# Kernel tuning notes

Hardware: AMD Instinct MI355X
Metric: run time of the kernel (lower is better)

The kernel has to match this reference:

```python
import jax, jax.numpy as jnp
import numpy as np

H = 400   # hidden_size
V = 77    # vocab / window size
K = 10    # attention mixture components
OUT = 121
B, T, U = 64, 600, 50


def setup_inputs() -> dict:
    key = jax.random.key(0)
    ks = jax.random.split(key, 16)
    def p(k, shape, s=0.08):
        return jax.random.normal(k, shape, dtype=jnp.float32) * s
    # bias for kappa-increment chunk kept negative so kappa advances ~exp(-3)=0.05/step
    b_win = jnp.concatenate([jnp.zeros(2 * K, jnp.float32), jnp.full((K,), -3.0, jnp.float32)])
    return {
        "inputs": jax.random.normal(ks[0], (B, T, 3), dtype=jnp.float32),
        "text": jax.random.randint(ks[1], (B, U), 0, V),
        "text_mask": jnp.ones((B, U), jnp.float32),
        "h0": jnp.zeros((3, B, H), jnp.float32),
        "c0": jnp.zeros((3, B, H), jnp.float32),
        "prev_window_vec": jnp.zeros((B, 1, V), jnp.float32),
        "prev_kappa": jnp.zeros((B, K, 1), jnp.float32),
        "w_ih1": p(ks[2], (4 * H, 3 + V)), "w_hh1": p(ks[3], (4 * H, H)),
        "b_ih1": jnp.zeros((4 * H,), jnp.float32), "b_hh1": jnp.zeros((4 * H,), jnp.float32),
        "w_ih2": p(ks[4], (4 * H, 3 + V + H)), "w_hh2": p(ks[5], (4 * H, H)),
        "b_ih2": jnp.zeros((4 * H,), jnp.float32), "b_hh2": jnp.zeros((4 * H,), jnp.float32),
        "w_ih3": p(ks[6], (4 * H, 3 + V + H)), "w_hh3": p(ks[7], (4 * H, H)),
        "b_ih3": jnp.zeros((4 * H,), jnp.float32), "b_hh3": jnp.zeros((4 * H,), jnp.float32),
        "w_win": p(ks[8], (3 * K, H), 0.01), "b_win": b_win,
        "w_out": p(ks[9], (OUT, 3 * H)), "b_out": jnp.zeros((OUT,), jnp.float32),
    }


def lstm_cell(x, h, c, Wih, Whh, bih, bhh):
    # PyTorch gate order: i, f, g, o
    g = x @ Wih.T + bih + h @ Whh.T + bhh
    i, f, gg, o = jnp.split(g, 4, axis=-1)
    c = jax.nn.sigmoid(f) * c + jax.nn.sigmoid(i) * jnp.tanh(gg)
    h = jax.nn.sigmoid(o) * jnp.tanh(c)
    return h, c


def reference(inputs, text, text_mask, h0, c0, prev_window_vec, prev_kappa,
              w_ih1, w_hh1, b_ih1, b_hh1, w_ih2, w_hh2, b_ih2, b_hh2,
              w_ih3, w_hh3, b_ih3, b_hh3, w_win, b_win, w_out, b_out):
    enc = jax.nn.one_hot(text, V, dtype=jnp.float32)            # [B,U,V]
    u = jnp.arange(U, dtype=jnp.float32)                         # [U]

    def step1(carry, x_t):
        h, c, wv, kappa = carry                                  # h,c:[B,H] wv:[B,V] kappa:[B,K]
        xi = jnp.concatenate([x_t, wv], axis=-1)                 # [B,3+V]
        h, c = lstm_cell(xi, h, c, w_ih1, w_hh1, b_ih1, b_hh1)
        mix = jnp.exp(h @ w_win.T + b_win)                       # [B,3K]
        alpha, beta, dk = jnp.split(mix, 3, axis=-1)             # each [B,K]
        kappa = kappa + dk
        phi = jnp.sum(alpha[:, :, None] * jnp.exp(-beta[:, :, None] * (kappa[:, :, None] - u) ** 2), axis=1)  # [B,U]
        phi = phi * text_mask
        wv = jnp.einsum('bu,buv->bv', phi, enc)                  # [B,V]
        return (h, c, wv, kappa), (h, wv)

    carry0 = (h0[0], c0[0], prev_window_vec[:, 0, :], prev_kappa[:, :, 0])
    (h1, c1, _, kappa_last), (hid1, wvec) = jax.lax.scan(step1, carry0, jnp.swapaxes(inputs, 0, 1))
    hid1 = jnp.swapaxes(hid1, 0, 1)                              # [B,T,H]
    wvec = jnp.swapaxes(wvec, 0, 1)                              # [B,T,V]

    def run_lstm(x, h, c, Wih, Whh, bih, bhh):
        def step(carry, x_t):
            h, c = carry
            h, c = lstm_cell(x_t, h, c, Wih, Whh, bih, bhh)
            return (h, c), h
        _, hs = jax.lax.scan(step, (h, c), jnp.swapaxes(x, 0, 1))
        return jnp.swapaxes(hs, 0, 1)

    hid2 = run_lstm(jnp.concatenate([inputs, hid1, wvec], axis=-1), h0[1], c0[1], w_ih2, w_hh2, b_ih2, b_hh2)
    hid3 = run_lstm(jnp.concatenate([inputs, hid2, wvec], axis=-1), h0[2], c0[2], w_ih3, w_hh3, b_ih3, b_hh3)
    y_hat = jnp.concatenate([hid1, hid2, hid3], axis=-1) @ w_out.T + b_out  # [B,T,121]
    return y_hat, wvec, kappa_last[:, :, None]
```

## Files before the change

kernel.cpp:

```cpp
#include <hip/hip_runtime.h>
#include <cstdint>
#include <cstddef>
#include <cstring>

using u32 = unsigned int;
typedef _Float16 h2 __attribute__((ext_vector_type(2)));
typedef _Float16 h4 __attribute__((ext_vector_type(4)));
typedef _Float16 h8 __attribute__((ext_vector_type(8)));
typedef float f32x4 __attribute__((ext_vector_type(4)));

constexpr int B_=64, T_=600, U_=50, V_=77, H_=400, OUT_=121;
constexpr int G1=50, GPA=16, G2=50, G3=50, GOUT=8;
constexpr int NBLK = G1+GPA+G2+G3+GOUT;

constexpr size_t FLAGS_B = 0;
constexpr size_t FLAGS_SZ = 4ull*600*64*16;
constexpr size_t W1WG   = 15ull*32*4*8;
constexpr size_t W1F_B  = FLAGS_SZ;
constexpr size_t W2WG   = 28ull*32*4*8;
constexpr size_t W2F_B  = W1F_B + 50ull*W1WG*2;
constexpr size_t W3F_B  = W2F_B + 50ull*W2WG*2;
constexpr size_t WOWG   = 300ull*32*16;
constexpr size_t WOF_B  = W3F_B + 50ull*W2WG*2;
constexpr size_t WWFWG  = 200ull*32;
constexpr size_t WWF_B  = WOF_B + 8ull*WOWG*2;
constexpr size_t WWMWG  = 15ull*32*4*8;
constexpr size_t WWM_B  = WWF_B + 16ull*WWFWG*4;
constexpr size_t FWV_B  = WWM_B + 50ull*WWMWG*2;
constexpr size_t FH1_B  = FWV_B + 600ull*64*40*4;
constexpr size_t FH2_B  = FH1_B + 600ull*64*200*4;
constexpr size_t FH3_B  = FH2_B + 600ull*64*200*4;

constexpr int SW1 = 184;
constexpr int SW2 = 232;
constexpr int SWO = 244;
constexpr int SMEM_BYTES = 59392;

struct P {
  const float *x, *tmask, *h0, *c0, *pwv, *pkap;
  const int *text;
  const float *wih1,*whh1,*bih1,*bhh1;
  const float *wih2,*whh2,*bih2,*bhh2;
  const float *wih3,*whh3,*bih3,*bhh3;
  const float *wwin,*bwin,*wout,*bout;
  float *out_y,*out_wv,*out_kap;
  _Float16 *w1f,*w2f,*w3f,*wof,*wwm;
  u32 *wwf;
  u32 *fwv,*fh1,*fh2,*fh3;
  u32 *flags;
};

__device__ __forceinline__ u32 ldc_u(const u32* p) {
  return __hip_atomic_load((u32*)p, __ATOMIC_RELAXED, __HIP_MEMORY_SCOPE_AGENT);
}
__device__ __forceinline__ void stc_u(u32* p, u32 v) {
  __hip_atomic_store(p, v, __ATOMIC_RELAXED, __HIP_MEMORY_SCOPE_AGENT);
}
__device__ __forceinline__ float sigm(float x) { return 1.f/(1.f+__expf(-x)); }
__device__ __forceinline__ h2 pk16(float a, float b) {
  auto t = __builtin_amdgcn_cvt_pkrtz(a, b);
  h2 r; memcpy(&r, &t, 4); return r;
}
__device__ __forceinline__ u32 h2u(h2 v) { u32 r; memcpy(&r, &v, 4); return r; }
__device__ __forceinline__ h2 u2h(u32 v) { h2 r; memcpy(&r, &v, 4); return r; }
__device__ __forceinline__ u32 pkf(float a, float b) { return h2u(pk16(a, b)); }
__device__ __forceinline__ float dot2(h2 a, h2 b, float c) { return __builtin_amdgcn_fdot2(a, b, c, false); }
__device__ __forceinline__ h2 lo4(h4 v) { return __builtin_shufflevector(v, v, 0, 1); }
__device__ __forceinline__ h2 hi4(h4 v) { return __builtin_shufflevector(v, v, 2, 3); }

__device__ __forceinline__ void wait_flags(u32* f, int stage, int t, int n) {
  if ((int)threadIdx.x < n) {
    const u32* s = f + (((size_t)stage*600 + t)*64 + threadIdx.x)*4;
    while (ldc_u(s) == 0) __builtin_amdgcn_s_sleep(2);
  }
  __syncthreads();
}
__device__ __forceinline__ void set_flag(u32* f, int stage, int t, int prod) {
  if (threadIdx.x == 0)
    stc_u(f + (((size_t)stage*600 + t)*64 + prod)*4, 1u);
}

__device__ __forceinline__ void mfma_chunk5(const _Float16* pan, int SWf, const _Float16* WA,
                                            int w, int l, f32x4& acc0, f32x4& acc1) {
  const _Float16* bp0 = pan + ((w>>1)*32 + (l&15))*SWf + (l>>4)*8;
  const _Float16* bp1 = bp0 + 16*SWf;
  const _Float16* ap  = WA + (((16*(w&1) + (l&15))*4) + (l>>4))*8;
#pragma unroll
  for (int ks = 0; ks < 5; ++ks) {
    h8 a  = *(const h8*)(ap  + ks*1024);
    h8 b0 = *(const h8*)(bp0 + ks*32);
    h8 b1 = *(const h8*)(bp1 + ks*32);
    acc0 = __builtin_amdgcn_mfma_f32_16x16x32_f16(a, b0, acc0, 0, 0, 0);
    acc1 = __builtin_amdgcn_mfma_f32_16x16x32_f16(a, b1, acc1, 0, 0, 0);
  }
}
__device__ __forceinline__ void mfma_chunk7(const _Float16* pan, int SWf, const _Float16* WA,
                                            int w, int l, f32x4& acc0, f32x4& acc1) {
  const _Float16* bp0 = pan + ((w>>1)*32 + (l&15))*SWf + (l>>4)*8;
  const _Float16* bp1 = bp0 + 16*SWf;
  const _Float16* ap  = WA + (((16*(w&1) + (l&15))*4) + (l>>4))*8;
#pragma unroll
  for (int ks = 0; ks < 7; ++ks) {
    h8 a  = *(const h8*)(ap  + ks*1024);
    h8 b0 = *(const h8*)(bp0 + ks*32);
    h8 b1 = *(const h8*)(bp1 + ks*32);
    acc0 = __builtin_amdgcn_mfma_f32_16x16x32_f16(a, b0, acc0, 0, 0, 0);
    acc1 = __builtin_amdgcn_mfma_f32_16x16x32_f16(a, b1, acc1, 0, 0, 0);
  }
}

__device__ void lstm1_role(const P& p, int wg, char* smem) {
  const int tid = threadIdx.x;
  const int w = tid >> 6, l = tid & 63;
  const int ul = (w&1)*4 + (l>>4);
  const int u  = wg*8 + ul;
  const int bA = (w>>1)*32 + (l&15), bB = bA + 16;
  _Float16* panA = (_Float16*)smem;
  _Float16* panB = panA + 64*SW1;
  float* kapS = (float*)(smem + 47104);
  float* mixE = (float*)(smem + 49664);
  float* wvs  = (float*)(smem + 23552);
  _Float16* wgW = p.w1f + (size_t)wg * W1WG;
  _Float16* wgM = p.wwm + (size_t)wg * WWMWG;
  for (int e = tid; e < 15360; e += 256) {
    int i = e & 7, q = (e>>3)&3, row = (e>>5)&31, ks = e>>10;
    int k = ks*32 + q*8 + i;
    int cu = row>>2, g = row&3;
    int r = g*400 + wg*8 + cu;
    float v;
    if (k < 400)      v = p.whh1[(size_t)r*400 + k];
    else if (k < 477) v = p.wih1[(size_t)r*80 + 3 + (k-400)];
    else              v = p.wih1[(size_t)r*80 + (k-477)];
    wgW[e] = (_Float16)v;
  }
  for (int e = tid; e < 15360; e += 256) {
    int i = e & 7, q = (e>>3)&3, row = (e>>5)&31, ks = e>>10;
    int k = ks*32 + q*8 + i;
    float v = 0.f;
    if (row < 30 && k < 400) v = p.wwin[(size_t)row*400 + k];
    wgM[e] = (_Float16)v;
  }
  for (int i = tid; i < 640; i += 256) kapS[i] = p.pkap[i];
  float bsum[4];
#pragma unroll
  for (int g = 0; g < 4; ++g) bsum[g] = p.bih1[g*400+u] + p.bhh1[g*400+u];
  float creg[2];
  creg[0] = p.c0[(size_t)bA*H_ + u];
  creg[1] = p.c0[(size_t)bB*H_ + u];
  __syncthreads();

  for (int t = 0; t < T_; ++t) {
    f32x4 acc0 = {0.f,0.f,0.f,0.f}, acc1 = {0.f,0.f,0.f,0.f};
    f32x4 am0  = {0.f,0.f,0.f,0.f}, am1  = {0.f,0.f,0.f,0.f};
    if (t > 0) wait_flags(p.flags, 0, t-1, G1); else __syncthreads();
    const u32* h1p = p.fh1 + (size_t)(t-1)*64*200;
    {
      u32 tmp[20];
#pragma unroll
      for (int it = 0; it < 20; ++it) {
        int idx = tid + it*256; int b = idx/80, q = idx - b*80;
        if (t == 0) { float2 f = *(const float2*)(p.h0 + (size_t)b*H_ + 2*q); tmp[it] = pkf(f.x, f.y); }
        else tmp[it] = h1p[b*200 + q];
      }
#pragma unroll
      for (int it = 0; it < 20; ++it) {
        int idx = tid + it*256; int b = idx/80, q = idx - b*80;
        ((u32*)panA)[b*92 + q] = tmp[it];
      }
    }
    __syncthreads();
    {
      u32 tmp[20];
#pragma unroll
      for (int it = 0; it < 20; ++it) {
        int idx = tid + it*256; int b = idx/80, q = 80 + (idx - b*80);
        if (t == 0) { float2 f = *(const float2*)(p.h0 + (size_t)b*H_ + 2*q); tmp[it] = pkf(f.x, f.y); }
        else tmp[it] = h1p[b*200 + q];
      }
      mfma_chunk5(panA, SW1, wgW, w, l, acc0, acc1);
      if (t > 0) mfma_chunk5(panA, SW1, wgM, w, l, am0, am1);
#pragma unroll
      for (int it = 0; it < 20; ++it) {
        int idx = tid + it*256; int b = idx/80, q = idx - b*80;
        ((u32*)panB)[b*92 + q] = tmp[it];
      }
    }
    __syncthreads();
    {
      u32 tmp[10], tw[10];
#pragma unroll
      for (int it = 0; it < 10; ++it) {
        int idx = tid + it*256; int b = idx/40, q = idx - b*40;
        if (t == 0) { float2 f = *(const float2*)(p.h0 + (size_t)b*H_ + 2*(160+q)); tmp[it] = pkf(f.x, f.y); }
        else tmp[it] = h1p[b*200 + 160 + q];
        if (t == 0) {
          u32 v;
          if (q < 38)       v = pkf(p.pwv[(size_t)b*V_ + 2*q], p.pwv[(size_t)b*V_ + 2*q + 1]);
          else if (q == 38) v = pkf(p.pwv[(size_t)b*V_ + 76], p.x[((size_t)b*T_ + t)*3 + 0]);
          else              v = pkf(p.x[((size_t)b*T_ + t)*3 + 1], p.x[((size_t)b*T_ + t)*3 + 2]);
          tw[it] = v;
        } else tw[it] = 0u;
      }
      mfma_chunk5(panB, SW1, wgW + 5*1024, w, l, acc0, acc1);
      if (t > 0) mfma_chunk5(panB, SW1, wgM + 5*1024, w, l, am0, am1);
#pragma unroll
      for (int it = 0; it < 10; ++it) {
        int idx = tid + it*256; int b = idx/40, q = idx - b*40;
        ((u32*)panA)[b*92 + q] = tmp[it];
        ((u32*)panA)[b*92 + 40 + q] = tw[it];
      }
    }
    __syncthreads();
    if (t > 0) {
      for (int i = tid; i < 4928; i += 256) wvs[i] = 0.f;
      mfma_chunk5(panA, SW1, wgM + 10*1024, w, l, am0, am1);
#pragma unroll
      for (int r = 0; r < 4; ++r) {
        int m = 16*(w&1) + (l>>4)*4 + r;
        if (m < 30) {
          float e0 = __expf(am0[r] + p.bwin[m]);
          float e1 = __expf(am1[r] + p.bwin[m]);
          mixE[bA*32 + m] = e0;
          mixE[bB*32 + m] = e1;
          if (m >= 20) { kapS[bA*10 + (m-20)] += e0; kapS[bB*10 + (m-20)] += e1; }
        }
      }
      __syncthreads();
      for (int c = tid; c < 3200; c += 256) {
        int b = c/50, uu = c - (c/50)*50;
        const float fu = (float)uu;
        float s = 0.f;
#pragma unroll
        for (int k = 0; k < 10; ++k) {
          float df = kapS[b*10+k] - fu;
          s += mixE[b*32+k] * __expf(-mixE[b*32+10+k]*df*df);
        }
        s *= p.tmask[(size_t)b*U_ + uu];
        atomicAdd(&wvs[b*77 + p.text[(size_t)b*U_ + uu]], s);
      }
      __syncthreads();
      for (int i = tid; i < 2560; i += 256) {
        int b = i/40, q = i - (i/40)*40;
        u32 v;
        if (q < 38)       v = pkf(wvs[b*77 + 2*q], wvs[b*77 + 2*q + 1]);
        else if (q == 38) v = pkf(wvs[b*77 + 76], p.x[((size_t)b*T_ + t)*3 + 0]);
        else              v = pkf(p.x[((size_t)b*T_ + t)*3 + 1], p.x[((size_t)b*T_ + t)*3 + 2]);
        ((u32*)panA)[b*92 + 40 + q] = v;
      }
      __syncthreads();
    }
    mfma_chunk5(panA, SW1, wgW + 10*1024, w, l, acc0, acc1);

    float hA, hB;
    {
      float cn = sigm(acc0[1]+bsum[1])*creg[0] + sigm(acc0[0]+bsum[0])*tanhf(acc0[2]+bsum[2]);
      creg[0] = cn; hA = sigm(acc0[3]+bsum[3])*tanhf(cn);
      float cn2 = sigm(acc1[1]+bsum[1])*creg[1] + sigm(acc1[0]+bsum[0])*tanhf(acc1[2]+bsum[2]);
      creg[1] = cn2; hB = sigm(acc1[3]+bsum[3])*tanhf(cn2);
    }
    {
      float hAp = __shfl_xor(hA, 16, 64);
      float hBp = __shfl_xor(hB, 16, 64);
      if (((l>>4) & 1) == 0) {
        const int pi = wg*4 + (ul>>1);
        stc_u(p.fh1 + ((size_t)t*64 + bA)*200 + pi, pkf(hA, hAp));
        stc_u(p.fh1 + ((size_t)t*64 + bB)*200 + pi, pkf(hB, hBp));
      }
    }
    __syncthreads();
    set_flag(p.flags, 0, t, wg);
  }
}

__device__ void pa_role(const P& p, int pa, char* smem) {
  const int tid = threadIdx.x;
  const int b0p = pa*4;
  u32* hsm    = (u32*)smem;
  float* mixP = (float*)(smem + 3200);
  float* mixL = (float*)(smem + 4160);
  float* kapL = (float*)(smem + 4640);
  float* wvs  = (float*)(smem + 4800);
  int* textL  = (int*)(smem + 6032);
  u32* wwf = p.wwf + (size_t)pa * WWFWG;
  for (int e = tid; e < 200*30; e += 256) {
    int kk = e / 30, m = e - (e/30)*30;
    wwf[(size_t)kk*32 + m] = pkf(p.wwin[(size_t)m*400 + 2*kk], p.wwin[(size_t)m*400 + 2*kk + 1]);
  }
  for (int i = tid; i < 200; i += 256)
    textL[i] = p.text[(size_t)(b0p + i/50)*U_ + (i - (i/50)*50)];
  float kap_reg = 0.f;
  if (tid < 120 && (tid % 30) >= 20)
    kap_reg = p.pkap[(size_t)(b0p + tid/30)*10 + (tid % 30 - 20)];
  __syncthreads();

  for (int t = 0; t < T_; ++t) {
    wait_flags(p.flags, 0, t, G1);
    for (int e = tid; e < 800; e += 256) {
      int bl = e / 200, q = e - bl*200;
      hsm[e] = p.fh1[((size_t)t*64 + b0p + bl)*200 + q];
    }
    for (int i = tid; i < 308; i += 256) wvs[i] = 0.f;
    __syncthreads();
    if (tid < 240) {
      int pp = tid >> 1, h = tid & 1;
      int bl = pp / 30, m = pp - bl*30;
      const u32* hp = hsm + bl*200 + h*100;
      const u32* wp = wwf + (size_t)(h*100)*32 + m;
      float d0=0.f, d1=0.f, d2=0.f, d3=0.f;
#pragma unroll 4
      for (int kk = 0; kk < 100; kk += 4) {
        d0 = dot2(u2h(hp[kk]),   u2h(wp[(size_t)kk*32]),     d0);
        d1 = dot2(u2h(hp[kk+1]), u2h(wp[(size_t)(kk+1)*32]), d1);
        d2 = dot2(u2h(hp[kk+2]), u2h(wp[(size_t)(kk+2)*32]), d2);
        d3 = dot2(u2h(hp[kk+3]), u2h(wp[(size_t)(kk+3)*32]), d3);
      }
      mixP[tid] = (d0+d1)+(d2+d3);
    }
    __syncthreads();
    if (tid < 120) {
      int bl = tid / 30, m = tid - bl*30;
      float v = __expf(mixP[2*tid] + mixP[2*tid+1] + p.bwin[m]);
      mixL[tid] = v;
      if (m >= 20) {
        kap_reg += v;
        kapL[bl*10 + (m-20)] = kap_reg;
        if (t == T_-1) p.out_kap[(size_t)(b0p+bl)*10 + (m-20)] = kap_reg;
      }
    }
    __syncthreads();
    if (tid < 200) {
      int bl = tid / 50, uu = tid - bl*50;
      const float fu = (float)uu;
      float s = 0.f;
#pragma unroll
      for (int k = 0; k < 10; ++k) {
        float df = kapL[bl*10+k] - fu;
        s += mixL[bl*30+k] * __expf(-mixL[bl*30+10+k]*df*df);
      }
      s *= p.tmask[(size_t)(b0p+bl)*U_ + uu];
      atomicAdd(&wvs[bl*77 + textL[tid]], s);
    }
    __syncthreads();
    for (int i = tid; i < 308; i += 256) {
      int bl = i / 77, v = i - (i/77)*77;
      p.out_wv[((size_t)(b0p+bl)*T_ + t)*V_ + v] = wvs[i];
    }
    for (int i = tid; i < 160; i += 256) {
      int bl = i / 40, pr = i - (i/40)*40;
      int b = b0p + bl;
      float f0, f1;
      if (pr < 38)       { f0 = wvs[bl*77 + 2*pr]; f1 = wvs[bl*77 + 2*pr + 1]; }
      else if (pr == 38) { f0 = wvs[bl*77 + 76];   f1 = p.x[((size_t)b*T_ + t)*3 + 0]; }
      else               { f0 = p.x[((size_t)b*T_ + t)*3 + 1]; f1 = p.x[((size_t)b*T_ + t)*3 + 2]; }
      stc_u(p.fwv + ((size_t)t*64 + b)*40 + pr, pkf(f0, f1));
    }
    __syncthreads();
    set_flag(p.flags, 1, t, pa);
  }
}

__device__ __forceinline__ void stage_l23(u32* pan, int tid, int ph, int t,
    const u32* fwvt, const u32* hint, const u32* rect, const float* h0f) {
  u32 tmp[28];
#pragma unroll
  for (int it = 0; it < 28; ++it) {
    int idx = tid + it*256;
    int b = idx/112, pl = idx - b*112;
    int gp = ph*112 + pl;
    u32 v;
    if (gp < 40) v = fwvt[b*40 + gp];
    else if (gp < 240) v = hint[b*200 + gp - 40];
    else if (gp < 440) {
      if (t == 0) { float2 f = *(const float2*)(h0f + (size_t)b*H_ + 2*(gp-240)); v = pkf(f.x, f.y); }
      else v = rect[b*200 + gp - 240];
    } else v = 0u;
    tmp[it] = v;
  }
#pragma unroll
  for (int it = 0; it < 28; ++it) {
    int idx = tid + it*256;
    int b = idx/112, pl = idx - b*112;
    pan[b*116 + pl] = tmp[it];
  }
}

template <int L>
__device__ void lstm_role(const P& p, int wg, char* smem) {
  const int tid = threadIdx.x;
  const int w = tid >> 6, l = tid & 63;
  const int ul = (w&1)*4 + (l>>4);
  const int u  = wg*8 + ul;
  const int bA = (w>>1)*32 + (l&15), bB = bA + 16;
  constexpr int STG = (L==2) ? 2 : 3;
  _Float16* wgW = ((L==2) ? p.w2f : p.w3f) + (size_t)wg * W2WG;
  const float* wih = (L==2) ? p.wih2 : p.wih3;
  const float* whh = (L==2) ? p.whh2 : p.whh3;
  const float* bih = (L==2) ? p.bih2 : p.bih3;
  const float* bhh = (L==2) ? p.bhh2 : p.bhh3;
  const u32* hin = (L==2) ? p.fh1 : p.fh2;
  u32* rec = (L==2) ? p.fh2 : p.fh3;
  _Float16* panA = (_Float16*)smem;
  _Float16* panB = panA + 64*SW2;

  for (int e = tid; e < 28672; e += 256) {
    int i = e & 7, q = (e>>3)&3, row = (e>>5)&31, ks = e>>10;
    int k = ks*32 + q*8 + i;
    int cu = row>>2, g = row&3;
    int r = g*400 + wg*8 + cu;
    float v;
    if (k < 77)       v = wih[(size_t)r*480 + 403 + k];
    else if (k < 80)  v = wih[(size_t)r*480 + (k-77)];
    else if (k < 480) v = wih[(size_t)r*480 + 3 + (k-80)];
    else if (k < 880) v = whh[(size_t)r*400 + (k-480)];
    else              v = 0.f;
    wgW[e] = (_Float16)v;
  }
  float bsum[4];
#pragma unroll
  for (int g = 0; g < 4; ++g) bsum[g] = bih[g*400+u] + bhh[g*400+u];
  float creg[2];
  creg[0] = p.c0[(size_t)(L-1)*B_*H_ + (size_t)bA*H_ + u];
  creg[1] = p.c0[(size_t)(L-1)*B_*H_ + (size_t)bB*H_ + u];
  __syncthreads();

  for (int t = 0; t < T_; ++t) {
    f32x4 acc0 = {0.f,0.f,0.f,0.f}, acc1 = {0.f,0.f,0.f,0.f};
    if (L == 2) wait_flags(p.flags, 1, t, GPA);
    else        wait_flags(p.flags, 2, t, G2);
    const u32* fwvt = p.fwv + (size_t)t*64*40;
    const u32* hint = hin + (size_t)t*64*200;
    const u32* rect = rec + (size_t)(t-1)*64*200;
    const float* h0f = p.h0 + (size_t)(L-1)*B_*H_;
    stage_l23((u32*)panA, tid, 0, t, fwvt, hint, rect, h0f);
    __syncthreads();
    {
      u32 tmp[28];
#pragma unroll
      for (int it = 0; it < 28; ++it) {
        int idx = tid + it*256;
        int b = idx/112, pl = idx - b*112;
        tmp[it] = hint[b*200 + 72 + pl];
      }
      mfma_chunk7(panA, SW2, wgW, w, l, acc0, acc1);
#pragma unroll
      for (int it = 0; it < 28; ++it) {
        int idx = tid + it*256;
        int b = idx/112, pl = idx - b*112;
        ((u32*)panB)[b*116 + pl] = tmp[it];
      }
    }
    if (t > 0) wait_flags(p.flags, STG, t-1, (L==2)?G2:G3); else __syncthreads();
    {
      u32 tmp[28];
#pragma unroll
      for (int it = 0; it < 28; ++it) {
        int idx = tid + it*256;
        int b = idx/112, pl = idx - b*112;
        int gp = 224 + pl;
        u32 v;
        if (gp < 240) v = hint[b*200 + gp - 40];
        else if (t == 0) { float2 f = *(const float2*)(h0f + (size_t)b*H_ + 2*(gp-240)); v = pkf(f.x, f.y); }
        else v = rect[b*200 + gp - 240];
        tmp[it] = v;
      }
      mfma_chunk7(panB, SW2, wgW + 7*1024, w, l, acc0, acc1);
#pragma unroll
      for (int it = 0; it < 28; ++it) {
        int idx = tid + it*256;
        int b = idx/112, pl = idx - b*112;
        ((u32*)panA)[b*116 + pl] = tmp[it];
      }
    }
    __syncthreads();
    {
      u32 tmp[28];
#pragma unroll
      for (int it = 0; it < 28; ++it) {
        int idx = tid + it*256;
        int b = idx/112, pl = idx - b*112;
        int gp = 336 + pl;
        u32 v;
        if (gp < 440) {
          if (t == 0) { float2 f = *(const float2*)(h0f + (size_t)b*H_ + 2*(gp-240)); v = pkf(f.x, f.y); }
          else v = rect[b*200 + gp - 240];
        } else v = 0u;
        tmp[it] = v;
      }
      mfma_chunk7(panA, SW2, wgW + 14*1024, w, l, acc0, acc1);
#pragma unroll
      for (int it = 0; it < 28; ++it) {
        int idx = tid + it*256;
        int b = idx/112, pl = idx - b*112;
        ((u32*)panB)[b*116 + pl] = tmp[it];
      }
    }
    __syncthreads();
    mfma_chunk7(panB, SW2, wgW + 21*1024, w, l, acc0, acc1);

    float hA, hB;
    {
      float cn = sigm(acc0[1]+bsum[1])*creg[0] + sigm(acc0[0]+bsum[0])*tanhf(acc0[2]+bsum[2]);
      creg[0] = cn; hA = sigm(acc0[3]+bsum[3])*tanhf(cn);
      float cn2 = sigm(acc1[1]+bsum[1])*creg[1] + sigm(acc1[0]+bsum[0])*tanhf(acc1[2]+bsum[2]);
      creg[1] = cn2; hB = sigm(acc1[3]+bsum[3])*tanhf(cn2);
    }
    {
      float hAp = __shfl_xor(hA, 16, 64);
      float hBp = __shfl_xor(hB, 16, 64);
      if (((l>>4) & 1) == 0) {
        const int pi = wg*4 + (ul>>1);
        stc_u(rec + ((size_t)t*64 + bA)*200 + pi, pkf(hA, hAp));
        stc_u(rec + ((size_t)t*64 + bB)*200 + pi, pkf(hB, hBp));
      }
    }
    __syncthreads();
    set_flag(p.flags, STG, t, wg);
  }
}

__device__ void out_role(const P& p, int g, char* smem) {
  const int tid = threadIdx.x;
  const int cg = tid & 31, bg = tid >> 5;
  const int c0 = cg*4;
  _Float16* pan = (_Float16*)smem;
  _Float16* wofg = p.wof + (size_t)g*WOWG;
  for (int e = tid; e < 300*32*16; e += 256) {
    int kk = e >> 9, rem = e & 511;
    int cgi = rem >> 4, j4 = rem & 15;
    int j = j4 >> 2, kc = j4 & 3;
    int c = cgi*4 + j; if (c > 120) c = 120;
    wofg[e] = (_Float16)p.wout[(size_t)c*1200 + kk*4 + kc];
  }
  float bo[4];
#pragma unroll
  for (int j = 0; j < 4; ++j) {
    int c = c0 + j; if (c > 120) c = 120;
    bo[j] = p.bout[c];
  }
  __syncthreads();

  for (int t = g; t < T_; t += GOUT) {
    wait_flags(p.flags, 3, t, G3);
    float acc[8][4];
#pragma unroll
    for (int r = 0; r < 8; ++r)
#pragma unroll
      for (int j = 0; j < 4; ++j) acc[r][j] = 0.f;

    for (int ph = 0; ph < 5; ++ph) {
      for (int idx = tid; idx < 7680; idx += 256) {
        int b = idx / 120, pl = idx - b*120;
        int Pp = ph*120 + pl;
        u32 pv;
        if (Pp < 200)      pv = p.fh1[((size_t)t*64 + b)*200 + Pp];
        else if (Pp < 400) pv = p.fh2[((size_t)t*64 + b)*200 + (Pp-200)];
        else               pv = p.fh3[((size_t)t*64 + b)*200 + (Pp-400)];
        ((u32*)pan)[b*122 + pl] = pv;
      }
      __syncthreads();
      const _Float16* wp = wofg + ((size_t)(ph*60)*32 + cg)*16;
#pragma unroll 3
      for (int k = 0; k < 240; k += 4) {
        h4 wa = *(const h4*)(wp);
        h4 wb = *(const h4*)(wp+4);
        h4 wc = *(const h4*)(wp+8);
        h4 wd = *(const h4*)(wp+12);
        wp += 512;
#pragma unroll
        for (int r = 0; r < 8; ++r) {
          h4 a = *(const h4*)(pan + (bg*8+r)*SWO + k);
          h2 al = lo4(a), ah = hi4(a);
          acc[r][0] = dot2(al, lo4(wa), acc[r][0]); acc[r][0] = dot2(ah, hi4(wa), acc[r][0]);
          acc[r][1] = dot2(al, lo4(wb), acc[r][1]); acc[r][1] = dot2(ah, hi4(wb), acc[r][1]);
          acc[r][2] = dot2(al, lo4(wc), acc[r][2]); acc[r][2] = dot2(ah, hi4(wc), acc[r][2]);
          acc[r][3] = dot2(al, lo4(wd), acc[r][3]); acc[r][3] = dot2(ah, hi4(wd), acc[r][3]);
        }
      }
      __syncthreads();
    }
#pragma unroll
    for (int r = 0; r < 8; ++r)
#pragma unroll
      for (int j = 0; j < 4; ++j) {
        int c = c0 + j;
        if (c < 121)
          p.out_y[((size_t)(bg*8+r)*T_ + t)*OUT_ + c] = acc[r][j] + bo[j];
      }
    __syncthreads();
  }
}

__global__ __launch_bounds__(256) void hw_pipeline(P p) {
  __shared__ __align__(16) char smem_raw[SMEM_BYTES];
  const int bid = blockIdx.x;
  if (bid < G1) lstm1_role(p, bid, smem_raw);
  else if (bid < G1+GPA) pa_role(p, bid - G1, smem_raw);
  else if (bid < G1+GPA+G2) lstm_role<2>(p, bid - G1 - GPA, smem_raw);
  else if (bid < G1+GPA+G2+G3) lstm_role<3>(p, bid - G1 - GPA - G2, smem_raw);
  else out_role(p, bid - G1 - GPA - G2 - G3, smem_raw);
}

extern "C" void kernel_launch(void* const* d_in, const int* in_sizes, int n_in,
                              void* d_out, int out_size, void* d_ws, size_t ws_size,
                              hipStream_t stream) {
  (void)in_sizes; (void)n_in; (void)out_size; (void)ws_size;
  P p;
  p.x = (const float*)d_in[0];
  p.text = (const int*)d_in[1];
  p.tmask = (const float*)d_in[2];
  p.h0 = (const float*)d_in[3];
  p.c0 = (const float*)d_in[4];
  p.pwv = (const float*)d_in[5];
  p.pkap = (const float*)d_in[6];
  p.wih1 = (const float*)d_in[7];  p.whh1 = (const float*)d_in[8];
  p.bih1 = (const float*)d_in[9];  p.bhh1 = (const float*)d_in[10];
  p.wih2 = (const float*)d_in[11]; p.whh2 = (const float*)d_in[12];
  p.bih2 = (const float*)d_in[13]; p.bhh2 = (const float*)d_in[14];
  p.wih3 = (const float*)d_in[15]; p.whh3 = (const float*)d_in[16];
  p.bih3 = (const float*)d_in[17]; p.bhh3 = (const float*)d_in[18];
  p.wwin = (const float*)d_in[19]; p.bwin = (const float*)d_in[20];
  p.wout = (const float*)d_in[21]; p.bout = (const float*)d_in[22];
  float* out = (float*)d_out;
  p.out_y  = out;
  p.out_wv = out + (size_t)B_*T_*OUT_;
  p.out_kap = p.out_wv + (size_t)B_*T_*V_;
  char* ws = (char*)d_ws;
  p.flags = (u32*)(ws + FLAGS_B);
  p.w1f = (_Float16*)(ws + W1F_B);
  p.w2f = (_Float16*)(ws + W2F_B);
  p.w3f = (_Float16*)(ws + W3F_B);
  p.wof = (_Float16*)(ws + WOF_B);
  p.wwm = (_Float16*)(ws + WWM_B);
  p.wwf = (u32*)(ws + WWF_B);
  p.fwv = (u32*)(ws + FWV_B);
  p.fh1 = (u32*)(ws + FH1_B);
  p.fh2 = (u32*)(ws + FH2_B);
  p.fh3 = (u32*)(ws + FH3_B);
  (void)hipMemsetAsync(ws + FLAGS_B, 0, FLAGS_SZ, stream);
  hipLaunchKernelGGL(hw_pipeline, dim3(NBLK), dim3(256), 0, stream, p);
}
```

Measured before the change: 14.51 ms.

## Transpose inter-stage hidden-state buffers to feature-major, batch-minor layout

Changes the global exchange buffers (fh1/fh2/fh3/fwv) from [t][batch][feature] to [t][feature][batch]. Producers write and consumers read with batch as the fastest index, so adjacent lanes touch adjacent addresses and index math becomes shifts instead of divides. The aim is more coalesced global traffic on the latency-critical per-step handoff between pipeline stages. The trade-off is scattered LDS writes into the batch-major panels, which may add bank conflicts, and the small stc_u stores in the producers become strided.

```diff
diff --git a/kernel.cpp b/kernel.cpp
--- a/kernel.cpp
+++ b/kernel.cpp
@@ -27,9 +27,11 @@
 constexpr size_t WWMWG  = 15ull*32*4*8;
 constexpr size_t WWM_B  = WWF_B + 16ull*WWFWG*4;
 constexpr size_t FWV_B  = WWM_B + 50ull*WWMWG*2;
-constexpr size_t FH1_B  = FWV_B + 600ull*64*40*4;
-constexpr size_t FH2_B  = FH1_B + 600ull*64*200*4;
-constexpr size_t FH3_B  = FH2_B + 600ull*64*200*4;
+constexpr size_t FH1_B  = FWV_B + 600ull*40*64*4;
+constexpr size_t FH2_B  = FH1_B + 600ull*200*64*4;
+constexpr size_t FH3_B  = FH2_B + 600ull*200*64*4;
+constexpr int FH_T = 200*64;
+constexpr int FWV_T = 40*64;
 
 constexpr int SW1 = 184;
 constexpr int SW2 = 232;
@@ -153,18 +155,18 @@
     f32x4 acc0 = {0.f,0.f,0.f,0.f}, acc1 = {0.f,0.f,0.f,0.f};
     f32x4 am0  = {0.f,0.f,0.f,0.f}, am1  = {0.f,0.f,0.f,0.f};
     if (t > 0) wait_flags(p.flags, 0, t-1, G1); else __syncthreads();
-    const u32* h1p = p.fh1 + (size_t)(t-1)*64*200;
+    const u32* h1p = p.fh1 + (size_t)(t-1)*FH_T;
     {
       u32 tmp[20];
 #pragma unroll
       for (int it = 0; it < 20; ++it) {
-        int idx = tid + it*256; int b = idx/80, q = idx - b*80;
+        int idx = tid + it*256; int q = idx>>6, b = idx&63;
         if (t == 0) { float2 f = *(const float2*)(p.h0 + (size_t)b*H_ + 2*q); tmp[it] = pkf(f.x, f.y); }
-        else tmp[it] = h1p[b*200 + q];
+        else tmp[it] = h1p[q*64 + b];
       }
 #pragma unroll
       for (int it = 0; it < 20; ++it) {
-        int idx = tid + it*256; int b = idx/80, q = idx - b*80;
+        int idx = tid + it*256; int q = idx>>6, b = idx&63;
         ((u32*)panA)[b*92 + q] = tmp[it];
       }
     }
@@ -173,15 +175,15 @@
       u32 tmp[20];
 #pragma unroll
       for (int it = 0; it < 20; ++it) {
-        int idx = tid + it*256; int b = idx/80, q = 80 + (idx - b*80);
-        if (t == 0) { float2 f = *(const float2*)(p.h0 + (size_t)b*H_ + 2*q); tmp[it] = pkf(f.x, f.y); }
-        else tmp[it] = h1p[b*200 + q];
+        int idx = tid + it*256; int q = idx>>6, b = idx&63;
+        if (t == 0) { float2 f = *(const float2*)(p.h0 + (size_t)b*H_ + 2*(80+q)); tmp[it] = pkf(f.x, f.y); }
+        else tmp[it] = h1p[(80+q)*64 + b];
       }
       mfma_chunk5(panA, SW1, wgW, w, l, acc0, acc1);
       if (t > 0) mfma_chunk5(panA, SW1, wgM, w, l, am0, am1);
 #pragma unroll
       for (int it = 0; it < 20; ++it) {
-        int idx = tid + it*256; int b = idx/80, q = idx - b*80;
+        int idx = tid + it*256; int q = idx>>6, b = idx&63;
         ((u32*)panB)[b*92 + q] = tmp[it];
       }
     }
@@ -190,9 +192,9 @@
       u32 tmp[10], tw[10];
 #pragma unroll
       for (int it = 0; it < 10; ++it) {
-        int idx = tid + it*256; int b = idx/40, q = idx - b*40;
+        int idx = tid + it*256; int q = idx>>6, b = idx&63;
         if (t == 0) { float2 f = *(const float2*)(p.h0 + (size_t)b*H_ + 2*(160+q)); tmp[it] = pkf(f.x, f.y); }
-        else tmp[it] = h1p[b*200 + 160 + q];
+        else tmp[it] = h1p[(160+q)*64 + b];
         if (t == 0) {
           u32 v;
           if (q < 38)       v = pkf(p.pwv[(size_t)b*V_ + 2*q], p.pwv[(size_t)b*V_ + 2*q + 1]);
@@ -205,7 +207,7 @@
       if (t > 0) mfma_chunk5(panB, SW1, wgM + 5*1024, w, l, am0, am1);
 #pragma unroll
       for (int it = 0; it < 10; ++it) {
-        int idx = tid + it*256; int b = idx/40, q = idx - b*40;
+        int idx = tid + it*256; int q = idx>>6, b = idx&63;
         ((u32*)panA)[b*92 + q] = tmp[it];
         ((u32*)panA)[b*92 + 40 + q] = tw[it];
       }
@@ -263,8 +265,8 @@
       float hBp = __shfl_xor(hB, 16, 64);
       if (((l>>4) & 1) == 0) {
         const int pi = wg*4 + (ul>>1);
-        stc_u(p.fh1 + ((size_t)t*64 + bA)*200 + pi, pkf(hA, hAp));
-        stc_u(p.fh1 + ((size_t)t*64 + bB)*200 + pi, pkf(hB, hBp));
+        stc_u(p.fh1 + (size_t)t*FH_T + pi*64 + bA, pkf(hA, hAp));
+        stc_u(p.fh1 + (size_t)t*FH_T + pi*64 + bB, pkf(hB, hBp));
       }
     }
     __syncthreads();
@@ -296,8 +298,8 @@
   for (int t = 0; t < T_; ++t) {
     wait_flags(p.flags, 0, t, G1);
     for (int e = tid; e < 800; e += 256) {
-      int bl = e / 200, q = e - bl*200;
-      hsm[e] = p.fh1[((size_t)t*64 + b0p + bl)*200 + q];
+      int q = e >> 2, bl = e & 3;
+      hsm[bl*200 + q] = p.fh1[(size_t)t*FH_T + q*64 + b0p + bl];
     }
     for (int i = tid; i < 308; i += 256) wvs[i] = 0.f;
     __syncthreads();
@@ -346,13 +348,13 @@
       p.out_wv[((size_t)(b0p+bl)*T_ + t)*V_ + v] = wvs[i];
     }
     for (int i = tid; i < 160; i += 256) {
-      int bl = i / 40, pr = i - (i/40)*40;
+      int pr = i >> 2, bl = i & 3;
       int b = b0p + bl;
       float f0, f1;
       if (pr < 38)       { f0 = wvs[bl*77 + 2*pr]; f1 = wvs[bl*77 + 2*pr + 1]; }
       else if (pr == 38) { f0 = wvs[bl*77 + 76];   f1 = p.x[((size_t)b*T_ + t)*3 + 0]; }
       else               { f0 = p.x[((size_t)b*T_ + t)*3 + 1]; f1 = p.x[((size_t)b*T_ + t)*3 + 2]; }
-      stc_u(p.fwv + ((size_t)t*64 + b)*40 + pr, pkf(f0, f1));
+      stc_u(p.fwv + (size_t)t*FWV_T + pr*64 + b, pkf(f0, f1));
     }
     __syncthreads();
     set_flag(p.flags, 1, t, pa);
@@ -365,21 +367,21 @@
 #pragma unroll
   for (int it = 0; it < 28; ++it) {
     int idx = tid + it*256;
-    int b = idx/112, pl = idx - b*112;
+    int pl = idx>>6, b = idx&63;
     int gp = ph*112 + pl;
     u32 v;
-    if (gp < 40) v = fwvt[b*40 + gp];
-    else if (gp < 240) v = hint[b*200 + gp - 40];
+    if (gp < 40) v = fwvt[gp*64 + b];
+    else if (gp < 240) v = hint[(gp-40)*64 + b];
     else if (gp < 440) {
       if (t == 0) { float2 f = *(const float2*)(h0f + (size_t)b*H_ + 2*(gp-240)); v = pkf(f.x, f.y); }
-      else v = rect[b*200 + gp - 240];
+      else v = rect[(gp-240)*64 + b];
     } else v = 0u;
     tmp[it] = v;
   }
 #pragma unroll
   for (int it = 0; it < 28; ++it) {
     int idx = tid + it*256;
-    int b = idx/112, pl = idx - b*112;
+    int pl = idx>>6, b = idx&63;
     pan[b*116 + pl] = tmp[it];
   }
 }
@@ -427,9 +429,9 @@
     f32x4 acc0 = {0.f,0.f,0.f,0.f}, acc1 = {0.f,0.f,0.f,0.f};
     if (L == 2) wait_flags(p.flags, 1, t, GPA);
     else        wait_flags(p.flags, 2, t, G2);
-    const u32* fwvt = p.fwv + (size_t)t*64*40;
-    const u32* hint = hin + (size_t)t*64*200;
-    const u32* rect = rec + (size_t)(t-1)*64*200;
+    const u32* fwvt = p.fwv + (size_t)t*FWV_T;
+    const u32* hint = hin + (size_t)t*FH_T;
+    const u32* rect = rec + (size_t)(t-1)*FH_T;
     const float* h0f = p.h0 + (size_t)(L-1)*B_*H_;
     stage_l23((u32*)panA, tid, 0, t, fwvt, hint, rect, h0f);
     __syncthreads();
@@ -438,14 +440,14 @@
 #pragma unroll
       for (int it = 0; it < 28; ++it) {
         int idx = tid + it*256;
-        int b = idx/112, pl = idx - b*112;
-        tmp[it] = hint[b*200 + 72 + pl];
+        int pl = idx>>6, b = idx&63;
+        tmp[it] = hint[(72+pl)*64 + b];
       }
       mfma_chunk7(panA, SW2, wgW, w, l, acc0, acc1);
 #pragma unroll
       for (int it = 0; it < 28; ++it) {
         int idx = tid + it*256;
-        int b = idx/112, pl = idx - b*112;
+        int pl = idx>>6, b = idx&63;
         ((u32*)panB)[b*116 + pl] = tmp[it];
       }
     }
@@ -455,19 +457,19 @@
 #pragma unroll
       for (int it = 0; it < 28; ++it) {
         int idx = tid + it*256;
-        int b = idx/112, pl = idx - b*112;
+        int pl = idx>>6, b = idx&63;
         int gp = 224 + pl;
         u32 v;
-        if (gp < 240) v = hint[b*200 + gp - 40];
+        if (gp < 240) v = hint[(gp-40)*64 + b];
         else if (t == 0) { float2 f = *(const float2*)(h0f + (size_t)b*H_ + 2*(gp-240)); v = pkf(f.x, f.y); }
-        else v = rect[b*200 + gp - 240];
+        else v = rect[(gp-240)*64 + b];
         tmp[it] = v;
       }
       mfma_chunk7(panB, SW2, wgW + 7*1024, w, l, acc0, acc1);
 #pragma unroll
       for (int it = 0; it < 28; ++it) {
         int idx = tid + it*256;
-        int b = idx/112, pl = idx - b*112;
+        int pl = idx>>6, b = idx&63;
         ((u32*)panA)[b*116 + pl] = tmp[it];
       }
     }
@@ -477,12 +479,12 @@
 #pragma unroll
       for (int it = 0; it < 28; ++it) {
         int idx = tid + it*256;
-        int b = idx/112, pl = idx - b*112;
+        int pl = idx>>6, b = idx&63;
         int gp = 336 + pl;
         u32 v;
         if (gp < 440) {
           if (t == 0) { float2 f = *(const float2*)(h0f + (size_t)b*H_ + 2*(gp-240)); v = pkf(f.x, f.y); }
-          else v = rect[b*200 + gp - 240];
+          else v = rect[(gp-240)*64 + b];
         } else v = 0u;
         tmp[it] = v;
       }
@@ -490,7 +492,7 @@
 #pragma unroll
       for (int it = 0; it < 28; ++it) {
         int idx = tid + it*256;
-        int b = idx/112, pl = idx - b*112;
+        int pl = idx>>6, b = idx&63;
         ((u32*)panB)[b*116 + pl] = tmp[it];
       }
     }
@@ -509,8 +511,8 @@
       float hBp = __shfl_xor(hB, 16, 64);
       if (((l>>4) & 1) == 0) {
         const int pi = wg*4 + (ul>>1);
-        stc_u(rec + ((size_t)t*64 + bA)*200 + pi, pkf(hA, hAp));
-        stc_u(rec + ((size_t)t*64 + bB)*200 + pi, pkf(hB, hBp));
+        stc_u(rec + (size_t)t*FH_T + pi*64 + bA, pkf(hA, hAp));
+        stc_u(rec + (size_t)t*FH_T + pi*64 + bB, pkf(hB, hBp));
       }
     }
     __syncthreads();
@@ -549,12 +551,12 @@
 
     for (int ph = 0; ph < 5; ++ph) {
       for (int idx = tid; idx < 7680; idx += 256) {
-        int b = idx / 120, pl = idx - b*120;
+        int pl = idx>>6, b = idx&63;
         int Pp = ph*120 + pl;
         u32 pv;
-        if (Pp < 200)      pv = p.fh1[((size_t)t*64 + b)*200 + Pp];
-        else if (Pp < 400) pv = p.fh2[((size_t)t*64 + b)*200 + (Pp-200)];
-        else               pv = p.fh3[((size_t)t*64 + b)*200 + (Pp-400)];
+        if (Pp < 200)      pv = p.fh1[(size_t)t*FH_T + Pp*64 + b];
+        else if (Pp < 400) pv = p.fh2[(size_t)t*FH_T + (Pp-200)*64 + b];
+        else               pv = p.fh3[(size_t)t*FH_T + (Pp-400)*64 + b];
         ((u32*)pan)[b*122 + pl] = pv;
       }
       __syncthreads();
```

New measurement: 13.60 ms. 1.07x faster.
